# Kernel optimization log

Measured on AMD Instinct MI355X. Metric: run time of the kernel, lower is better.

## Reference

```python
import jax, jax.numpy as jnp
import numpy as np

N_A = 100000
N_B = 100000
D = 128
E = 400000


def setup_inputs() -> dict:
    key = jax.random.key(0)
    ks = jax.random.split(key, 14)
    inp = {
        'x_A': jax.random.normal(ks[0], (N_A, D), dtype=jnp.float32),
        'x_B': jax.random.normal(ks[1], (N_B, D), dtype=jnp.float32),
        'W_msg_ab1': jax.random.normal(ks[2], (D, D), dtype=jnp.float32) / np.sqrt(D),
        'W_self_ab1': jax.random.normal(ks[3], (D, D), dtype=jnp.float32) / np.sqrt(D),
        'W_msg_ab2': jax.random.normal(ks[4], (D, D), dtype=jnp.float32) / np.sqrt(D),
        'W_self_ab2': jax.random.normal(ks[5], (D, D), dtype=jnp.float32) / np.sqrt(D),
        'W_msg_ba': jax.random.normal(ks[6], (D, D), dtype=jnp.float32) / np.sqrt(D),
        'W_self_ba': jax.random.normal(ks[7], (D, D), dtype=jnp.float32) / np.sqrt(D),
        'src_ab1': jax.random.randint(ks[8], (E,), 0, N_A, dtype=jnp.int32),
        'dst_ab1': jax.random.randint(ks[9], (E,), 0, N_B, dtype=jnp.int32),
        'src_ab2': jax.random.randint(ks[10], (E,), 0, N_A, dtype=jnp.int32),
        'dst_ab2': jax.random.randint(ks[11], (E,), 0, N_B, dtype=jnp.int32),
        'src_ba': jax.random.randint(ks[12], (E,), 0, N_B, dtype=jnp.int32),
        'dst_ba': jax.random.randint(ks[13], (E,), 0, N_A, dtype=jnp.int32),
    }
    return inp


def _conv(x_src, x_dst, src_idx, dst_idx, num_dst, W_msg, W_self):
    # gather -> transform -> scatter-add, plus dst self-transform
    msg = x_src[src_idx] @ W_msg                              # [E, D]
    agg = jax.ops.segment_sum(msg, dst_idx, num_segments=num_dst)  # [num_dst, D]
    return agg + x_dst @ W_self


def reference(x_A, x_B,
              W_msg_ab1, W_self_ab1, W_msg_ab2, W_self_ab2,
              W_msg_ba, W_self_ba,
              src_ab1, dst_ab1, src_ab2, dst_ab2, src_ba, dst_ba):
    # two edge types with dst_type B are accumulated (out_dict[dst] + result)
    out_B = _conv(x_A, x_B, src_ab1, dst_ab1, N_B, W_msg_ab1, W_self_ab1) \
          + _conv(x_A, x_B, src_ab2, dst_ab2, N_B, W_msg_ab2, W_self_ab2)
    out_A = _conv(x_B, x_A, src_ba, dst_ba, N_A, W_msg_ba, W_self_ba)
    return out_A, out_B
```

## Files before the change

kernel.cpp:

```cpp
#include <hip/hip_runtime.h>

constexpr int D   = 128;
constexpr int NA  = 100000;
constexpr int NB  = 100000;
constexpr int NE  = 400000;
constexpr int CAP = 24;

typedef __attribute__((ext_vector_type(8))) short           bf16x8;
typedef __attribute__((ext_vector_type(4))) float           f32x4;
typedef __attribute__((ext_vector_type(4))) unsigned short  us4;

static __device__ __forceinline__ unsigned short f2bf(float f) {
    unsigned u = __float_as_uint(f);
    unsigned r = (u + 0x7FFFu + ((u >> 16) & 1u)) >> 16;
    return (unsigned short)r;
}

__global__ __launch_bounds__(256) void prep_weights_kernel(
    unsigned short* __restrict__ WT,
    const float* __restrict__ Wmba,  const float* __restrict__ Wsba,
    const float* __restrict__ Wmab1, const float* __restrict__ Wmab2,
    const float* __restrict__ Wsab1, const float* __restrict__ Wsab2)
{
    int idx = blockIdx.x * 256 + threadIdx.x;
    int m   = idx >> 14;
    int rem = idx & 16383;
    int c   = rem >> 7;
    int k   = rem & 127;
    float v;
    if      (m == 0) v = Wmba [k * D + c];
    else if (m == 1) v = Wsba [k * D + c];
    else if (m == 2) v = Wmab1[k * D + c];
    else if (m == 3) v = Wmab2[k * D + c];
    else             v = Wsab1[k * D + c] + Wsab2[k * D + c];
    WT[idx] = f2bf(v);
}

__global__ __launch_bounds__(256) void fill_kernel(
    int* __restrict__ cursor, int* __restrict__ slots,
    const int* __restrict__ src, const int* __restrict__ dst, int E)
{
    int e = blockIdx.x * 256 + threadIdx.x;
    if (e >= E) return;
    int d = dst[e];
    int pos = atomicAdd(&cursor[d], 1);
    if (pos < CAP) slots[(size_t)d * CAP + pos] = src[e];
}

__global__ __launch_bounds__(256) void gather_sum_kernel(
    unsigned short* __restrict__ G, const float* __restrict__ X,
    const int* __restrict__ cursor, const int* __restrict__ slots, int N)
{
    int t = blockIdx.x * 256 + threadIdx.x;
    int r = t >> 5;
    if (r >= N) return;
    int j = (t & 31) << 2;
    int deg = min(cursor[r], CAP);
    const int* sl = slots + (size_t)r * CAP;
    float4 acc0 = make_float4(0.f, 0.f, 0.f, 0.f);
    float4 acc1 = make_float4(0.f, 0.f, 0.f, 0.f);
    int i = 0;
    for (; i + 1 < deg; i += 2) {
        int s0 = sl[i], s1 = sl[i + 1];
        float4 v0 = *reinterpret_cast<const float4*>(X + (size_t)s0 * D + j);
        float4 v1 = *reinterpret_cast<const float4*>(X + (size_t)s1 * D + j);
        acc0.x += v0.x; acc0.y += v0.y; acc0.z += v0.z; acc0.w += v0.w;
        acc1.x += v1.x; acc1.y += v1.y; acc1.z += v1.z; acc1.w += v1.w;
    }
    if (i < deg) {
        int s0 = sl[i];
        float4 v0 = *reinterpret_cast<const float4*>(X + (size_t)s0 * D + j);
        acc0.x += v0.x; acc0.y += v0.y; acc0.z += v0.z; acc0.w += v0.w;
    }
    acc0.x += acc1.x; acc0.y += acc1.y; acc0.z += acc1.z; acc0.w += acc1.w;
    us4 o;
    o.x = f2bf(acc0.x); o.y = f2bf(acc0.y); o.z = f2bf(acc0.z); o.w = f2bf(acc0.w);
    *reinterpret_cast<us4*>(G + (size_t)r * D + j) = o;
}

template<int NBF>
__global__ __launch_bounds__(256) void mfma_gemm_kernel(
    float* __restrict__ out,
    const unsigned short* __restrict__ A0, const unsigned short* __restrict__ WT0,
    const unsigned short* __restrict__ A1, const unsigned short* __restrict__ WT1,
    const float* __restrict__ AS, const unsigned short* __restrict__ WTS,
    int N)
{
    const int tid  = threadIdx.x;
    const int lane = tid & 63;
    const int wid  = tid >> 6;
    const int g    = lane >> 4;
    const int m    = lane & 15;
    const int row_base = blockIdx.x * 128 + wid * 32;

    f32x4 acc[2][8];
    #pragma unroll
    for (int rt = 0; rt < 2; ++rt)
        #pragma unroll
        for (int ct = 0; ct < 8; ++ct)
            acc[rt][ct] = (f32x4){0.f, 0.f, 0.f, 0.f};

    #pragma unroll
    for (int p = 0; p < NBF; ++p) {
        const unsigned short* __restrict__ A = (p == 0) ? A0 : A1;
        const unsigned short* __restrict__ W = (p == 0) ? WT0 : WT1;
        bf16x8 af[2][4];
        #pragma unroll
        for (int rt = 0; rt < 2; ++rt) {
            int r = row_base + rt * 16 + m;
            r = (r < N) ? r : (N - 1);
            const unsigned short* ap = A + (size_t)r * D + g * 8;
            #pragma unroll
            for (int ks = 0; ks < 4; ++ks)
                af[rt][ks] = *reinterpret_cast<const bf16x8*>(ap + ks * 32);
        }
        #pragma unroll
        for (int ct = 0; ct < 8; ++ct) {
            const unsigned short* wp = W + (size_t)(ct * 16 + m) * D + g * 8;
            bf16x8 bf[4];
            #pragma unroll
            for (int ks = 0; ks < 4; ++ks)
                bf[ks] = *reinterpret_cast<const bf16x8*>(wp + ks * 32);
            #pragma unroll
            for (int ks = 0; ks < 4; ++ks) {
                acc[0][ct] = __builtin_amdgcn_mfma_f32_16x16x32_bf16(af[0][ks], bf[ks], acc[0][ct], 0, 0, 0);
                acc[1][ct] = __builtin_amdgcn_mfma_f32_16x16x32_bf16(af[1][ks], bf[ks], acc[1][ct], 0, 0, 0);
            }
        }
    }

    {
        bf16x8 af[2][4];
        #pragma unroll
        for (int rt = 0; rt < 2; ++rt) {
            int r = row_base + rt * 16 + m;
            r = (r < N) ? r : (N - 1);
            const float* ap = AS + (size_t)r * D + g * 8;
            #pragma unroll
            for (int ks = 0; ks < 4; ++ks) {
                float4 lo = *reinterpret_cast<const float4*>(ap + ks * 32);
                float4 hi = *reinterpret_cast<const float4*>(ap + ks * 32 + 4);
                bf16x8 f;
                f[0] = (short)f2bf(lo.x); f[1] = (short)f2bf(lo.y);
                f[2] = (short)f2bf(lo.z); f[3] = (short)f2bf(lo.w);
                f[4] = (short)f2bf(hi.x); f[5] = (short)f2bf(hi.y);
                f[6] = (short)f2bf(hi.z); f[7] = (short)f2bf(hi.w);
                af[rt][ks] = f;
            }
        }
        #pragma unroll
        for (int ct = 0; ct < 8; ++ct) {
            const unsigned short* wp = WTS + (size_t)(ct * 16 + m) * D + g * 8;
            bf16x8 bf[4];
            #pragma unroll
            for (int ks = 0; ks < 4; ++ks)
                bf[ks] = *reinterpret_cast<const bf16x8*>(wp + ks * 32);
            #pragma unroll
            for (int ks = 0; ks < 4; ++ks) {
                acc[0][ct] = __builtin_amdgcn_mfma_f32_16x16x32_bf16(af[0][ks], bf[ks], acc[0][ct], 0, 0, 0);
                acc[1][ct] = __builtin_amdgcn_mfma_f32_16x16x32_bf16(af[1][ks], bf[ks], acc[1][ct], 0, 0, 0);
            }
        }
    }

    #pragma unroll
    for (int rt = 0; rt < 2; ++rt) {
        #pragma unroll
        for (int ct = 0; ct < 8; ++ct) {
            int col = ct * 16 + m;
            int r0  = row_base + rt * 16 + g * 4;
            #pragma unroll
            for (int j = 0; j < 4; ++j) {
                int r = r0 + j;
                if (r < N) out[(size_t)r * D + col] = acc[rt][ct][j];
            }
        }
    }
}

extern "C" void kernel_launch(void* const* d_in, const int* in_sizes, int n_in,
                              void* d_out, int out_size, void* d_ws, size_t ws_size,
                              hipStream_t stream)
{
    const float* x_A        = (const float*)d_in[0];
    const float* x_B        = (const float*)d_in[1];
    const float* W_msg_ab1  = (const float*)d_in[2];
    const float* W_self_ab1 = (const float*)d_in[3];
    const float* W_msg_ab2  = (const float*)d_in[4];
    const float* W_self_ab2 = (const float*)d_in[5];
    const float* W_msg_ba   = (const float*)d_in[6];
    const float* W_self_ba  = (const float*)d_in[7];
    const int* src_ab1 = (const int*)d_in[8];
    const int* dst_ab1 = (const int*)d_in[9];
    const int* src_ab2 = (const int*)d_in[10];
    const int* dst_ab2 = (const int*)d_in[11];
    const int* src_ba  = (const int*)d_in[12];
    const int* dst_ba  = (const int*)d_in[13];

    float* out_A = (float*)d_out;
    float* out_B = out_A + (size_t)NA * D;

    char* ws = (char*)d_ws;
    unsigned short* G0 = (unsigned short*)ws;
    unsigned short* G1 = G0 + (size_t)NA * D;
    int* cursor = (int*)(G1 + (size_t)NA * D);
    int* slots  = cursor + NA;
    unsigned short* WT = (unsigned short*)(slots + (size_t)NA * CAP);
    unsigned short* WT_mba  = WT;
    unsigned short* WT_sba  = WT + 1 * D * D;
    unsigned short* WT_mab1 = WT + 2 * D * D;
    unsigned short* WT_mab2 = WT + 3 * D * D;
    unsigned short* WT_sab  = WT + 4 * D * D;

    const dim3 blk(256);
    const int fill_blocks = (NE + 255) / 256;
    const int gs_blocks   = (NA * 32) / 256;
    const int gm_blocks   = (NA + 127) / 128;
    const size_t cbytes   = (size_t)NA * sizeof(int);

    prep_weights_kernel<<<5 * D * D / 256, blk, 0, stream>>>(
        WT, W_msg_ba, W_self_ba, W_msg_ab1, W_msg_ab2, W_self_ab1, W_self_ab2);

    hipMemsetAsync(cursor, 0, cbytes, stream);
    fill_kernel<<<fill_blocks, blk, 0, stream>>>(cursor, slots, src_ba, dst_ba, NE);
    gather_sum_kernel<<<gs_blocks, blk, 0, stream>>>(G0, x_B, cursor, slots, NA);
    mfma_gemm_kernel<1><<<gm_blocks, blk, 0, stream>>>(
        out_A, G0, WT_mba, nullptr, nullptr, x_A, WT_sba, NA);

    hipMemsetAsync(cursor, 0, cbytes, stream);
    fill_kernel<<<fill_blocks, blk, 0, stream>>>(cursor, slots, src_ab1, dst_ab1, NE);
    gather_sum_kernel<<<gs_blocks, blk, 0, stream>>>(G0, x_A, cursor, slots, NB);
    hipMemsetAsync(cursor, 0, cbytes, stream);
    fill_kernel<<<fill_blocks, blk, 0, stream>>>(cursor, slots, src_ab2, dst_ab2, NE);
    gather_sum_kernel<<<gs_blocks, blk, 0, stream>>>(G1, x_A, cursor, slots, NB);
    mfma_gemm_kernel<2><<<gm_blocks, blk, 0, stream>>>(
        out_B, G0, WT_mab1, G1, WT_mab2, x_B, WT_sab, NB);
}
```

Before: 473.1 us.

## Fuse neighbor gather-sum into MFMA GEMM via swizzled LDS tile

```diff
diff --git a/kernel.cpp b/kernel.cpp
--- a/kernel.cpp
+++ b/kernel.cpp
@@ -47,133 +47,128 @@
     if (pos < CAP) slots[(size_t)d * CAP + pos] = src[e];
 }
 
-__global__ __launch_bounds__(256) void gather_sum_kernel(
-    unsigned short* __restrict__ G, const float* __restrict__ X,
-    const int* __restrict__ cursor, const int* __restrict__ slots, int N)
-{
-    int t = blockIdx.x * 256 + threadIdx.x;
-    int r = t >> 5;
-    if (r >= N) return;
-    int j = (t & 31) << 2;
-    int deg = min(cursor[r], CAP);
-    const int* sl = slots + (size_t)r * CAP;
-    float4 acc0 = make_float4(0.f, 0.f, 0.f, 0.f);
-    float4 acc1 = make_float4(0.f, 0.f, 0.f, 0.f);
-    int i = 0;
-    for (; i + 1 < deg; i += 2) {
-        int s0 = sl[i], s1 = sl[i + 1];
-        float4 v0 = *reinterpret_cast<const float4*>(X + (size_t)s0 * D + j);
-        float4 v1 = *reinterpret_cast<const float4*>(X + (size_t)s1 * D + j);
-        acc0.x += v0.x; acc0.y += v0.y; acc0.z += v0.z; acc0.w += v0.w;
-        acc1.x += v1.x; acc1.y += v1.y; acc1.z += v1.z; acc1.w += v1.w;
-    }
-    if (i < deg) {
-        int s0 = sl[i];
-        float4 v0 = *reinterpret_cast<const float4*>(X + (size_t)s0 * D + j);
-        acc0.x += v0.x; acc0.y += v0.y; acc0.z += v0.z; acc0.w += v0.w;
-    }
-    acc0.x += acc1.x; acc0.y += acc1.y; acc0.z += acc1.z; acc0.w += acc1.w;
-    us4 o;
-    o.x = f2bf(acc0.x); o.y = f2bf(acc0.y); o.z = f2bf(acc0.z); o.w = f2bf(acc0.w);
-    *reinterpret_cast<us4*>(G + (size_t)r * D + j) = o;
-}
-
 template<int NBF>
-__global__ __launch_bounds__(256) void mfma_gemm_kernel(
+__global__ __launch_bounds__(256) void fused_gnn_kernel(
     float* __restrict__ out,
-    const unsigned short* __restrict__ A0, const unsigned short* __restrict__ WT0,
-    const unsigned short* __restrict__ A1, const unsigned short* __restrict__ WT1,
-    const float* __restrict__ AS, const unsigned short* __restrict__ WTS,
+    const float* __restrict__ XM,
+    const int* __restrict__ cur0, const int* __restrict__ sl0,
+    const int* __restrict__ cur1, const int* __restrict__ sl1,
+    const float* __restrict__ XS,
+    const unsigned short* __restrict__ WT0,
+    const unsigned short* __restrict__ WT1,
+    const unsigned short* __restrict__ WTS,
     int N)
 {
+    __shared__ unsigned short tile[NBF][64][128];
+
     const int tid  = threadIdx.x;
+    const int row0 = blockIdx.x * 64;
+
+    {
+        const int lj   = tid & 31;
+        const int rsub = tid >> 5;
+        #pragma unroll
+        for (int p = 0; p < NBF; ++p) {
+            const int* __restrict__ cur = (p == 0) ? cur0 : cur1;
+            const int* __restrict__ sl  = (p == 0) ? sl0  : sl1;
+            #pragma unroll
+            for (int it = 0; it < 8; ++it) {
+                int rl = it * 8 + rsub;
+                int r  = row0 + rl;
+                float4 a0 = make_float4(0.f, 0.f, 0.f, 0.f);
+                float4 a1 = make_float4(0.f, 0.f, 0.f, 0.f);
+                if (r < N) {
+                    int deg = min(cur[r], CAP);
+                    const int* s = sl + (size_t)r * CAP;
+                    int i = 0;
+                    for (; i + 1 < deg; i += 2) {
+                        int s0 = s[i], s1 = s[i + 1];
+                        float4 v0 = *reinterpret_cast<const float4*>(XM + (size_t)s0 * D + lj * 4);
+                        float4 v1 = *reinterpret_cast<const float4*>(XM + (size_t)s1 * D + lj * 4);
+                        a0.x += v0.x; a0.y += v0.y; a0.z += v0.z; a0.w += v0.w;
+                        a1.x += v1.x; a1.y += v1.y; a1.z += v1.z; a1.w += v1.w;
+                    }
+                    if (i < deg) {
+                        float4 v0 = *reinterpret_cast<const float4*>(XM + (size_t)s[i] * D + lj * 4);
+                        a0.x += v0.x; a0.y += v0.y; a0.z += v0.z; a0.w += v0.w;
+                    }
+                    a0.x += a1.x; a0.y += a1.y; a0.z += a1.z; a0.w += a1.w;
+                }
+                us4 o;
+                o.x = f2bf(a0.x); o.y = f2bf(a0.y); o.z = f2bf(a0.z); o.w = f2bf(a0.w);
+                int cb = (lj * 8) ^ ((rl & 7) << 4);
+                *reinterpret_cast<us4*>(reinterpret_cast<char*>(&tile[p][rl][0]) + cb) = o;
+            }
+        }
+    }
+    __syncthreads();
+
     const int lane = tid & 63;
     const int wid  = tid >> 6;
     const int g    = lane >> 4;
     const int m    = lane & 15;
-    const int row_base = blockIdx.x * 128 + wid * 32;
-
-    f32x4 acc[2][8];
+    const int rl0  = wid * 16;
+
+    f32x4 acc[8];
     #pragma unroll
-    for (int rt = 0; rt < 2; ++rt)
-        #pragma unroll
-        for (int ct = 0; ct < 8; ++ct)
-            acc[rt][ct] = (f32x4){0.f, 0.f, 0.f, 0.f};
+    for (int ct = 0; ct < 8; ++ct) acc[ct] = (f32x4){0.f, 0.f, 0.f, 0.f};
 
     #pragma unroll
     for (int p = 0; p < NBF; ++p) {
-        const unsigned short* __restrict__ A = (p == 0) ? A0 : A1;
+        bf16x8 af[4];
+        const char* rowp = reinterpret_cast<const char*>(&tile[p][rl0 + m][0]);
+        #pragma unroll
+        for (int ks = 0; ks < 4; ++ks) {
+            int cb = (g * 16 + ks * 64) ^ ((m & 7) << 4);
+            af[ks] = *reinterpret_cast<const bf16x8*>(rowp + cb);
+        }
         const unsigned short* __restrict__ W = (p == 0) ? WT0 : WT1;
-        bf16x8 af[2][4];
-        #pragma unroll
-        for (int rt = 0; rt < 2; ++rt) {
-            int r = row_base + rt * 16 + m;
-            r = (r < N) ? r : (N - 1);
-            const unsigned short* ap = A + (size_t)r * D + g * 8;
-            #pragma unroll
-            for (int ks = 0; ks < 4; ++ks)
-                af[rt][ks] = *reinterpret_cast<const bf16x8*>(ap + ks * 32);
-        }
         #pragma unroll
         for (int ct = 0; ct < 8; ++ct) {
             const unsigned short* wp = W + (size_t)(ct * 16 + m) * D + g * 8;
-            bf16x8 bf[4];
-            #pragma unroll
-            for (int ks = 0; ks < 4; ++ks)
-                bf[ks] = *reinterpret_cast<const bf16x8*>(wp + ks * 32);
             #pragma unroll
             for (int ks = 0; ks < 4; ++ks) {
-                acc[0][ct] = __builtin_amdgcn_mfma_f32_16x16x32_bf16(af[0][ks], bf[ks], acc[0][ct], 0, 0, 0);
-                acc[1][ct] = __builtin_amdgcn_mfma_f32_16x16x32_bf16(af[1][ks], bf[ks], acc[1][ct], 0, 0, 0);
+                bf16x8 bfv = *reinterpret_cast<const bf16x8*>(wp + ks * 32);
+                acc[ct] = __builtin_amdgcn_mfma_f32_16x16x32_bf16(af[ks], bfv, acc[ct], 0, 0, 0);
             }
         }
     }
 
     {
-        bf16x8 af[2][4];
-        #pragma unroll
-        for (int rt = 0; rt < 2; ++rt) {
-            int r = row_base + rt * 16 + m;
-            r = (r < N) ? r : (N - 1);
-            const float* ap = AS + (size_t)r * D + g * 8;
+        int r = row0 + rl0 + m;
+        r = (r < N) ? r : (N - 1);
+        const float* ap = XS + (size_t)r * D + g * 8;
+        bf16x8 af[4];
+        #pragma unroll
+        for (int ks = 0; ks < 4; ++ks) {
+            float4 lo = *reinterpret_cast<const float4*>(ap + ks * 32);
+            float4 hi = *reinterpret_cast<const float4*>(ap + ks * 32 + 4);
+            bf16x8 f;
+            f[0] = (short)f2bf(lo.x); f[1] = (short)f2bf(lo.y);
+            f[2] = (short)f2bf(lo.z); f[3] = (short)f2bf(lo.w);
+            f[4] = (short)f2bf(hi.x); f[5] = (short)f2bf(hi.y);
+            f[6] = (short)f2bf(hi.z); f[7] = (short)f2bf(hi.w);
+            af[ks] = f;
+        }
+        #pragma unroll
+        for (int ct = 0; ct < 8; ++ct) {
+            const unsigned short* wp = WTS + (size_t)(ct * 16 + m) * D + g * 8;
             #pragma unroll
             for (int ks = 0; ks < 4; ++ks) {
-                float4 lo = *reinterpret_cast<const float4*>(ap + ks * 32);
-                float4 hi = *reinterpret_cast<const float4*>(ap + ks * 32 + 4);
-                bf16x8 f;
-                f[0] = (short)f2bf(lo.x); f[1] = (short)f2bf(lo.y);
-                f[2] = (short)f2bf(lo.z); f[3] = (short)f2bf(lo.w);
-                f[4] = (short)f2bf(hi.x); f[5] = (short)f2bf(hi.y);
-                f[6] = (short)f2bf(hi.z); f[7] = (short)f2bf(hi.w);
-                af[rt][ks] = f;
+                bf16x8 bfv = *reinterpret_cast<const bf16x8*>(wp + ks * 32);
+                acc[ct] = __builtin_amdgcn_mfma_f32_16x16x32_bf16(af[ks], bfv, acc[ct], 0, 0, 0);
             }
         }
-        #pragma unroll
-        for (int ct = 0; ct < 8; ++ct) {
-            const unsigned short* wp = WTS + (size_t)(ct * 16 + m) * D + g * 8;
-            bf16x8 bf[4];
-            #pragma unroll
-            for (int ks = 0; ks < 4; ++ks)
-                bf[ks] = *reinterpret_cast<const bf16x8*>(wp + ks * 32);
-            #pragma unroll
-            for (int ks = 0; ks < 4; ++ks) {
-                acc[0][ct] = __builtin_amdgcn_mfma_f32_16x16x32_bf16(af[0][ks], bf[ks], acc[0][ct], 0, 0, 0);
-                acc[1][ct] = __builtin_amdgcn_mfma_f32_16x16x32_bf16(af[1][ks], bf[ks], acc[1][ct], 0, 0, 0);
-            }
-        }
-    }
-
+    }
+
+    const int r0 = row0 + rl0 + g * 4;
     #pragma unroll
-    for (int rt = 0; rt < 2; ++rt) {
-        #pragma unroll
-        for (int ct = 0; ct < 8; ++ct) {
-            int col = ct * 16 + m;
-            int r0  = row_base + rt * 16 + g * 4;
-            #pragma unroll
-            for (int j = 0; j < 4; ++j) {
-                int r = r0 + j;
-                if (r < N) out[(size_t)r * D + col] = acc[rt][ct][j];
-            }
+    for (int ct = 0; ct < 8; ++ct) {
+        int col = ct * 16 + m;
+        #pragma unroll
+        for (int j = 0; j < 4; ++j) {
+            int r = r0 + j;
+            if (r < N) out[(size_t)r * D + col] = acc[ct][j];
         }
     }
 }
@@ -201,11 +196,14 @@
     float* out_B = out_A + (size_t)NA * D;
 
     char* ws = (char*)d_ws;
-    unsigned short* G0 = (unsigned short*)ws;
-    unsigned short* G1 = G0 + (size_t)NA * D;
-    int* cursor = (int*)(G1 + (size_t)NA * D);
-    int* slots  = cursor + NA;
-    unsigned short* WT = (unsigned short*)(slots + (size_t)NA * CAP);
+    int* cur = (int*)ws;
+    int* cur0 = cur;
+    int* cur1 = cur + NA;
+    int* cur2 = cur + 2 * NA;
+    int* sl0 = cur + 3 * NA;
+    int* sl1 = sl0 + (size_t)NA * CAP;
+    int* sl2 = sl1 + (size_t)NA * CAP;
+    unsigned short* WT = (unsigned short*)(sl2 + (size_t)NA * CAP);
     unsigned short* WT_mba  = WT;
     unsigned short* WT_sba  = WT + 1 * D * D;
     unsigned short* WT_mab1 = WT + 2 * D * D;
@@ -214,25 +212,19 @@
 
     const dim3 blk(256);
     const int fill_blocks = (NE + 255) / 256;
-    const int gs_blocks   = (NA * 32) / 256;
-    const int gm_blocks   = (NA + 127) / 128;
-    const size_t cbytes   = (size_t)NA * sizeof(int);
+    const int gnn_blocks  = (NA + 63) / 64;
 
     prep_weights_kernel<<<5 * D * D / 256, blk, 0, stream>>>(
         WT, W_msg_ba, W_self_ba, W_msg_ab1, W_msg_ab2, W_self_ab1, W_self_ab2);
 
-    hipMemsetAsync(cursor, 0, cbytes, stream);
-    fill_kernel<<<fill_blocks, blk, 0, stream>>>(cursor, slots, src_ba, dst_ba, NE);
-    gather_sum_kernel<<<gs_blocks, blk, 0, stream>>>(G0, x_B, cursor, slots, NA);
-    mfma_gemm_kernel<1><<<gm_blocks, blk, 0, stream>>>(
-        out_A, G0, WT_mba, nullptr, nullptr, x_A, WT_sba, NA);
-
-    hipMemsetAsync(cursor, 0, cbytes, stream);
-    fill_kernel<<<fill_blocks, blk, 0, stream>>>(cursor, slots, src_ab1, dst_ab1, NE);
-    gather_sum_kernel<<<gs_blocks, blk, 0, stream>>>(G0, x_A, cursor, slots, NB);
-    hipMemsetAsync(cursor, 0, cbytes, stream);
-    fill_kernel<<<fill_blocks, blk, 0, stream>>>(cursor, slots, src_ab2, dst_ab2, NE);
-    gather_sum_kernel<<<gs_blocks, blk, 0, stream>>>(G1, x_A, cursor, slots, NB);
-    mfma_gemm_kernel<2><<<gm_blocks, blk, 0, stream>>>(
-        out_B, G0, WT_mab1, G1, WT_mab2, x_B, WT_sab, NB);
-}
+    hipMemsetAsync(cur, 0, 3 * (size_t)NA * sizeof(int), stream);
+    fill_kernel<<<fill_blocks, blk, 0, stream>>>(cur0, sl0, src_ba,  dst_ba,  NE);
+    fill_kernel<<<fill_blocks, blk, 0, stream>>>(cur1, sl1, src_ab1, dst_ab1, NE);
+    fill_kernel<<<fill_blocks, blk, 0, stream>>>(cur2, sl2, src_ab2, dst_ab2, NE);
+
+    fused_gnn_kernel<1><<<gnn_blocks, blk, 0, stream>>>(
+        out_A, x_B, cur0, sl0, nullptr, nullptr, x_A, WT_mba, nullptr, WT_sba, NA);
+
+    fused_gnn_kernel<2><<<gnn_blocks, blk, 0, stream>>>(
+        out_B, x_A, cur1, sl1, cur2, sl2, x_B, WT_mab1, WT_mab2, WT_sab, NB);
+}
```

Result: slower. 566.4 us (+19.7%).
